# Kernel tuning notes

Hardware: AMD Instinct MI355X
Metric: run time of the kernel (lower is better)

The kernel has to match this reference:

```python
import jax, jax.numpy as jnp
import numpy as np

B, S, HID = 1, 2048, 7168
QLORA = 1536
NH = 32          # index_n_heads
HD = 128         # index_head_dim
ROPE = 64        # qk_rope_head_dim
TOPK = 512       # index_topk
EPS = 1e-6
NEG = -1e9       # finite mask value -> deterministic top-k (no -inf ties)


def _rope(x, cos, sin):
    # non-interleaved rotary: x [b,s,h,d]; cos/sin [s, d//2]
    half = x.shape[-1] // 2
    x1, x2 = x[..., :half], x[..., half:]
    c = cos[None, :, None, :]
    s = sin[None, :, None, :]
    return jnp.concatenate([x1 * c - x2 * s, x1 * s + x2 * c], axis=-1)


def setup_inputs() -> dict:
    key = jax.random.key(0)
    ks = jax.random.split(key, 8)
    x = jax.random.normal(ks[0], (B, S, HID), jnp.float32)
    qr = jax.random.normal(ks[1], (B, S, QLORA), jnp.float32)
    # rotary tables, theta=10000
    inv = 1.0 / (10000.0 ** (np.arange(0, ROPE, 2, dtype=np.float32) / ROPE))
    ang = np.arange(S, dtype=np.float32)[:, None] * inv[None, :]   # [S, ROPE//2]
    freqs_cos = jnp.asarray(np.cos(ang))
    freqs_sin = jnp.asarray(np.sin(ang))
    # causal additive mask [S, S], broadcasts over batch on [b,t,s]
    tri = jnp.tril(jnp.ones((S, S), jnp.bool_))
    mask = jnp.where(tri, 0.0, NEG).astype(jnp.float32)
    wq_b = jax.random.normal(ks[2], (QLORA, NH * HD), jnp.float32) / np.sqrt(QLORA)
    wk = jax.random.normal(ks[3], (HID, HD), jnp.float32) / np.sqrt(HID)
    k_norm_w = jnp.ones((HD,), jnp.float32)
    w_weights = jax.random.normal(ks[4], (HID, NH), jnp.float32) / np.sqrt(HID)
    return {"x": x, "qr": qr, "freqs_cos": freqs_cos, "freqs_sin": freqs_sin,
            "mask": mask, "wq_b": wq_b, "wk": wk, "k_norm_w": k_norm_w,
            "w_weights": w_weights}


def reference(x, qr, freqs_cos, freqs_sin, mask, wq_b, wk, k_norm_w, w_weights):
    b, s, _ = x.shape
    # queries
    q = (qr @ wq_b).reshape(b, s, NH, HD)
    q_pe, q_nope = q[..., :ROPE], q[..., ROPE:]
    q_pe = _rope(q_pe, freqs_cos, freqs_sin)
    q = jnp.concatenate([q_pe, q_nope], axis=-1)            # [b,s,NH,HD]
    # keys: project + RMSNorm + rope on first ROPE dims
    k = x @ wk                                              # [b,s,HD]
    var = jnp.mean(k * k, axis=-1, keepdims=True)
    k = k_norm_w * (k * jax.lax.rsqrt(var + EPS))
    k_pe, k_nope = k[..., :ROPE], k[..., ROPE:]
    k_pe = _rope(k_pe[:, :, None, :], freqs_cos, freqs_sin)[:, :, 0, :]
    k = jnp.concatenate([k_pe, k_nope], axis=-1)            # [b,s,HD]
    # per-head query weights
    weights = (x @ w_weights) * (NH ** -0.5) * (HD ** -0.5)  # [b,s,NH]
    # relu scores and per-head weighted reduction
    logits = jax.nn.relu(jnp.einsum('bthd,bsd->btsh', q, k))  # [b,t,s,NH]
    score = jnp.einsum('btsh,bth->bts', logits, weights) + mask
    # top-k token selection -> additive index mask
    topk_idx = jax.lax.top_k(score, min(TOPK, s))[1]          # [b,t,k]
    bi = jnp.arange(b)[:, None, None]
    ti = jnp.arange(s)[None, :, None]
    out = jnp.full((b, s, s), -jnp.inf, dtype=x.dtype)
    out = out.at[bi, ti, topk_idx].set(0.0)
    return out
```

## Files before the change

kernel.cpp:

```cpp
#include <hip/hip_runtime.h>
#include <hip/hip_bf16.h>
#include <math.h>

#define S_LEN 2048
#define HID   7168
#define QLORA 1536
#define NH    32
#define HD    128
#define T0    512
#define MROWS 1536
#define NEGV  -1000000000.0f
#define EPSV  1e-6f
#define NEG_FILL -3.0e38f
#define KSPLIT 16
#define KCHUNK 448

typedef __attribute__((ext_vector_type(8))) short bf16x8;
typedef __attribute__((ext_vector_type(4))) float f32x4;

__device__ __forceinline__ unsigned short f2bf(float x) {
    __hip_bfloat16 h = __float2bfloat16(x);
    union { __hip_bfloat16 h; unsigned short u; } cv; cv.h = h; return cv.u;
}
__device__ __forceinline__ float bf2f(short u) {
    return __uint_as_float(((unsigned)(unsigned short)u) << 16);
}
__device__ __forceinline__ void gload_lds16(const void* gsrc, void* ldst) {
    __builtin_amdgcn_global_load_lds(
        (const __attribute__((address_space(1))) void*)gsrc,
        (__attribute__((address_space(3))) void*)ldst,
        16, 0, 0);
}

__global__ __launch_bounds__(256) void transpose_wqb(
    const float* __restrict__ B, unsigned short* __restrict__ BT)
{
    __shared__ float tbuf[64][65];
    const int tid = threadIdx.x;
    const int n0 = blockIdx.x * 64;
    const int k0 = blockIdx.y * 64;
    {
        int r = tid >> 2, c0 = (tid & 3) * 16;
        const float* src = &B[(size_t)(k0 + r) * 4096 + n0 + c0];
        #pragma unroll
        for (int i = 0; i < 4; ++i) {
            float4 v = *(const float4*)(src + 4 * i);
            tbuf[r][c0 + 4 * i]     = v.x;
            tbuf[r][c0 + 4 * i + 1] = v.y;
            tbuf[r][c0 + 4 * i + 2] = v.z;
            tbuf[r][c0 + 4 * i + 3] = v.w;
        }
    }
    __syncthreads();
    {
        int nn = tid >> 2, ks = (tid & 3) * 16;
        bf16x8 p0, p1;
        #pragma unroll
        for (int j = 0; j < 8; ++j) {
            p0[j] = (short)f2bf(tbuf[ks + j][nn]);
            p1[j] = (short)f2bf(tbuf[ks + 8 + j][nn]);
        }
        unsigned short* dst = &BT[(size_t)(n0 + nn) * QLORA + k0 + ks];
        *(bf16x8*)dst       = p0;
        *(bf16x8*)(dst + 8) = p1;
    }
}

__global__ __launch_bounds__(256) void transpose_w(
    const float* __restrict__ wk, const float* __restrict__ ww,
    unsigned short* __restrict__ wbT)
{
    __shared__ float tbuf[64][33];
    const int tid = threadIdx.x;
    const int k0 = blockIdx.x * 64;
    const int nt = blockIdx.y;
    const float* src; int ld, nc0;
    if (nt < 4) { src = wk; ld = HD; nc0 = nt * 32; }
    else        { src = ww; ld = NH; nc0 = 0; }
    {
        int r = tid >> 2, c0 = (tid & 3) * 8;
        const float* sp = &src[(size_t)(k0 + r) * ld + nc0 + c0];
        #pragma unroll
        for (int i = 0; i < 2; ++i) {
            float4 v = *(const float4*)(sp + 4 * i);
            tbuf[r][c0 + 4 * i]     = v.x;
            tbuf[r][c0 + 4 * i + 1] = v.y;
            tbuf[r][c0 + 4 * i + 2] = v.z;
            tbuf[r][c0 + 4 * i + 3] = v.w;
        }
    }
    __syncthreads();
    {
        int nn = tid >> 3, ks = (tid & 7) * 8;
        bf16x8 p;
        #pragma unroll
        for (int j = 0; j < 8; ++j) p[j] = (short)f2bf(tbuf[ks + j][nn]);
        *(bf16x8*)&wbT[(size_t)(nt * 32 + nn) * HID + k0 + ks] = p;
    }
}

__global__ __launch_bounds__(256) void cast_qr(
    const float* __restrict__ qr, unsigned short* __restrict__ qrb)
{
    int idx = blockIdx.x * 256 + threadIdx.x;
    const float* src = qr + (size_t)T0 * QLORA + (size_t)idx * 8;
    float4 f0 = *(const float4*)src;
    float4 f1 = *(const float4*)(src + 4);
    bf16x8 p;
    p[0]=(short)f2bf(f0.x); p[1]=(short)f2bf(f0.y); p[2]=(short)f2bf(f0.z); p[3]=(short)f2bf(f0.w);
    p[4]=(short)f2bf(f1.x); p[5]=(short)f2bf(f1.y); p[6]=(short)f2bf(f1.z); p[7]=(short)f2bf(f1.w);
    *(bf16x8*)(qrb + (size_t)idx * 8) = p;
}

__global__ __launch_bounds__(256) void kw_gemm2(
    const float* __restrict__ x, const unsigned short* __restrict__ wbT,
    unsigned short* __restrict__ P)
{
    __shared__ char As[2][4096];
    __shared__ char Bs[2][10240];
    const int tid = threadIdx.x;
    const int bid = blockIdx.x;
    const int wg = (bid & 7) * 64 + (bid >> 3);
    const int kc = wg >> 5;
    const int m0 = (wg & 31) * 64;
    const int kbase = kc * KCHUNK;
    const int wv = tid >> 6, l = tid & 63, g = l >> 4, r15 = l & 15;
    const int ar = tid >> 2, asub = tid & 3;
    f32x4 acc[10] = {};
    float4 fa, fb;

#define LOAD_A(kt) do {                                                          \
        const float* ap = &x[(size_t)(m0 + ar) * HID + kbase + (kt) * 32 + asub * 8]; \
        fa = *(const float4*)ap;  fb = *(const float4*)(ap + 4);                 \
    } while (0)
#define WRITE_A(buf) do {                                                        \
        bf16x8 pk;                                                               \
        pk[0]=(short)f2bf(fa.x); pk[1]=(short)f2bf(fa.y);                        \
        pk[2]=(short)f2bf(fa.z); pk[3]=(short)f2bf(fa.w);                        \
        pk[4]=(short)f2bf(fb.x); pk[5]=(short)f2bf(fb.y);                        \
        pk[6]=(short)f2bf(fb.z); pk[7]=(short)f2bf(fb.w);                        \
        *(bf16x8*)(As[buf] + (ar << 6) + ((asub ^ ((ar >> 1) & 3)) << 4)) = pk;  \
    } while (0)
#define STAGE_B(buf, kt) do {                                                    \
        int k0_ = kbase + (kt) * 32;                                             \
        { int slot = (wv << 6) + l;                                              \
          int n_ = slot >> 2, sub_ = (slot & 3) ^ ((n_ >> 1) & 3);               \
          gload_lds16(wbT + (size_t)n_ * HID + k0_ + sub_ * 8,                   \
                      Bs[buf] + (wv << 10)); }                                   \
        { int slot = 256 + (wv << 6) + l;                                        \
          int n_ = slot >> 2, sub_ = (slot & 3) ^ ((n_ >> 1) & 3);               \
          gload_lds16(wbT + (size_t)n_ * HID + k0_ + sub_ * 8,                   \
                      Bs[buf] + 4096 + (wv << 10)); }                            \
        if (wv < 2) {                                                            \
          int slot = 512 + (wv << 6) + l;                                        \
          int n_ = slot >> 2, sub_ = (slot & 3) ^ ((n_ >> 1) & 3);               \
          gload_lds16(wbT + (size_t)n_ * HID + k0_ + sub_ * 8,                   \
                      Bs[buf] + 8192 + (wv << 10)); }                            \
    } while (0)

    LOAD_A(0);
    STAGE_B(0, 0);
    WRITE_A(0);
    __syncthreads();
    int cur = 0;
    for (int t = 0; t < 14; ++t) {
        if (t < 13) { LOAD_A(t + 1); STAGE_B(cur ^ 1, t + 1); }
        {
            char* Ab = As[cur];
            char* Bb = Bs[cur];
            int ra = (wv << 4) + r15;
            bf16x8 a = *(const bf16x8*)(Ab + (ra << 6) + ((g ^ ((ra >> 1) & 3)) << 4));
            #pragma unroll
            for (int fn = 0; fn < 10; ++fn) {
                int nb = (fn << 4) + r15;
                bf16x8 b = *(const bf16x8*)(Bb + (nb << 6) + ((g ^ ((nb >> 1) & 3)) << 4));
                acc[fn] = __builtin_amdgcn_mfma_f32_16x16x32_bf16(a, b, acc[fn], 0, 0, 0);
            }
        }
        if (t < 13) WRITE_A(cur ^ 1);
        __syncthreads();
        cur ^= 1;
    }
#undef LOAD_A
#undef WRITE_A
#undef STAGE_B
    #pragma unroll
    for (int fn = 0; fn < 10; ++fn)
        #pragma unroll
        for (int rr = 0; rr < 4; ++rr) {
            int row = m0 + (wv << 4) + (g << 2) + rr;
            P[((size_t)kc * S_LEN + row) * 160 + (fn << 4) + r15] = f2bf(acc[fn][rr]);
        }
}

__global__ __launch_bounds__(512) void kw_finish16(
    const unsigned short* __restrict__ P, const float* __restrict__ knw,
    const float* __restrict__ fcos, const float* __restrict__ fsin,
    unsigned short* __restrict__ Kf, float* __restrict__ W)
{
    __shared__ float res[16][160];
    __shared__ float rsq[16];
    const int tid = threadIdx.x;
    const int stile = blockIdx.x;
    const int row0 = stile * 16;
    const int r = tid >> 5, j = tid & 31;

    #pragma unroll
    for (int jj = 0; jj < 5; ++jj) {
        int c = j + 32 * jj;
        float s = 0.f;
        #pragma unroll
        for (int kc = 0; kc < KSPLIT; ++kc)
            s += bf2f((short)P[(size_t)(kc * S_LEN + row0 + r) * 160 + c]);
        res[r][c] = s;
    }
    __syncthreads();
    {
        float s2 = 0.f;
        #pragma unroll
        for (int cg = 0; cg < 4; ++cg) { float v = res[r][cg * 32 + j]; s2 += v * v; }
        #pragma unroll
        for (int off = 16; off > 0; off >>= 1) s2 += __shfl_xor(s2, off, 32);
        if (j == 0) rsq[r] = rsqrtf(s2 * (1.0f / 128.0f) + EPSV);
    }
    __syncthreads();
    {
        int rr = tid >> 5, h = tid & 31;
        W[(size_t)(row0 + rr) * NH + h] = res[rr][128 + h] * 0.015625f;
    }
    if (tid < 256) {
        int ks = tid >> 6, l = tid & 63;
        int row = l & 15, g = l >> 4;
        int t = row0 + row;
        float rs = rsq[row];
        bf16x8 pack;
        #pragma unroll
        for (int jj2 = 0; jj2 < 8; ++jj2) {
            int d = ks * 32 + 8 * g + jj2;
            float v;
            if (d < 32) {
                float a = res[row][d]      * rs * knw[d];
                float b = res[row][d + 32] * rs * knw[d + 32];
                v = a * fcos[(size_t)t * 32 + d] - b * fsin[(size_t)t * 32 + d];
            } else if (d < 64) {
                int jx = d - 32;
                float a = res[row][jx] * rs * knw[jx];
                float b = res[row][d]  * rs * knw[d];
                v = a * fsin[(size_t)t * 32 + jx] + b * fcos[(size_t)t * 32 + jx];
            } else {
                v = res[row][d] * rs * knw[d];
            }
            pack[jj2] = (short)f2bf(v);
        }
        *(bf16x8*)&Kf[(size_t)stile * 2048 + ks * 512 + l * 8] = pack;
    }
}

__global__ __launch_bounds__(256) void gemm_q2(
    const unsigned short* __restrict__ qrb, const unsigned short* __restrict__ wqbT,
    const float* __restrict__ fcos, const float* __restrict__ fsin,
    unsigned short* __restrict__ Qbu)
{
    __shared__ char lds[2][12288];
    const int tid = threadIdx.x;
    const int bid = blockIdx.x;
    const int wg = (bid & 7) * 96 + (bid >> 3);
    const int n0 = (wg / 24) * 128;
    const int m0 = (wg % 24) * 64;
    const int wv = tid >> 6, l = tid & 63, g = l >> 4, r15 = l & 15;
    const int lrow = l >> 2, lsub = l & 3;
    const int wm = wv >> 1, wn = wv & 1;
    f32x4 acc[2][4] = {};

#define STAGE_Q(buf, kt) do {                                                   \
        int k0_ = (kt) * 32;                                                    \
        { int row_ = wv * 16 + lrow; int gs_ = lsub ^ ((row_ >> 1) & 3);        \
          gload_lds16(qrb + (size_t)(m0 + row_) * QLORA + k0_ + gs_ * 8,        \
                      lds[buf] + (wv << 10)); }                                 \
        { int row_ = wv * 32 + lrow; int gs_ = lsub ^ ((row_ >> 1) & 3);        \
          gload_lds16(wqbT + (size_t)(n0 + row_) * QLORA + k0_ + gs_ * 8,       \
                      lds[buf] + 4096 + (wv << 11)); }                          \
        { int row_ = wv * 32 + 16 + lrow; int gs_ = lsub ^ ((row_ >> 1) & 3);   \
          gload_lds16(wqbT + (size_t)(n0 + row_) * QLORA + k0_ + gs_ * 8,       \
                      lds[buf] + 4096 + (wv << 11) + 1024); }                   \
    } while (0)

    STAGE_Q(0, 0);
    __syncthreads();
    int cur = 0;
    for (int t = 0; t < 48; ++t) {
        if (t + 1 < 48) STAGE_Q(cur ^ 1, t + 1);
        char* As = lds[cur];
        char* Bs = lds[cur] + 4096;
        bf16x8 a[2], b[4];
        #pragma unroll
        for (int fm = 0; fm < 2; ++fm) {
            int ra = wm * 32 + fm * 16 + r15;
            a[fm] = *(const bf16x8*)(As + (ra << 6) + ((g ^ ((ra >> 1) & 3)) << 4));
        }
        #pragma unroll
        for (int fn = 0; fn < 4; ++fn) {
            int nb = wn * 64 + fn * 16 + r15;
            b[fn] = *(const bf16x8*)(Bs + (nb << 6) + ((g ^ ((nb >> 1) & 3)) << 4));
        }
        #pragma unroll
        for (int fm = 0; fm < 2; ++fm)
            #pragma unroll
            for (int fn = 0; fn < 4; ++fn)
                acc[fm][fn] = __builtin_amdgcn_mfma_f32_16x16x32_bf16(a[fm], b[fn], acc[fm][fn], 0, 0, 0);
        __syncthreads();
        cur ^= 1;
    }
#undef STAGE_Q
    if (wn == 0) {
        #pragma unroll
        for (int fm = 0; fm < 2; ++fm)
            #pragma unroll
            for (int rr = 0; rr < 4; ++rr) {
                int t = T0 + m0 + wm * 32 + fm * 16 + 4 * g + rr;
                #pragma unroll
                for (int p = 0; p < 2; ++p) {
                    int jj = p * 16 + r15;
                    float c = fcos[(size_t)t * 32 + jj];
                    float s = fsin[(size_t)t * 32 + jj];
                    float a = acc[fm][p][rr], b = acc[fm][p + 2][rr];
                    acc[fm][p][rr]     = a * c - b * s;
                    acc[fm][p + 2][rr] = a * s + b * c;
                }
            }
    }
    #pragma unroll
    for (int fm = 0; fm < 2; ++fm)
        #pragma unroll
        for (int fn = 0; fn < 4; ++fn)
            #pragma unroll
            for (int rr = 0; rr < 4; ++rr) {
                int row = m0 + wm * 32 + fm * 16 + 4 * g + rr;
                int col = n0 + wn * 64 + fn * 16 + r15;
                Qbu[(size_t)row * 4096 + col] = f2bf(acc[fm][fn][rr]);
            }
}

__global__ __launch_bounds__(512, 2) void score_mfma3(
    const unsigned short* __restrict__ Qb, const unsigned short* __restrict__ Kf,
    const float* __restrict__ W, float* __restrict__ sc)
{
    __shared__ float ps[2][8][320];
    __shared__ float wl2[32][16];
    const int tid = threadIdx.x;
    const int tt  = 95 - blockIdx.x;
    const int sp  = blockIdx.y;
    const int t0  = T0 + 16 * tt;
    const int wv  = tid >> 6, l = tid & 63, g = l >> 4, r15 = l & 15;

    {
        int h = tid >> 4, gg = (tid >> 2) & 3, r = tid & 3;
        wl2[h][gg * 4 + r] = W[(size_t)(t0 + 4 * gg + r) * NH + h];
    }
    bf16x8 qf[4][4];
    {
        const unsigned short* qbase = Qb + (size_t)(16 * tt + r15) * 4096 + g * 8;
        #pragma unroll
        for (int hh = 0; hh < 4; ++hh)
            #pragma unroll
            for (int ks = 0; ks < 4; ++ks)
                qf[hh][ks] = *(const bf16x8*)(qbase + (4 * wv + hh) * 128 + ks * 32);
    }
    __syncthreads();

    const int nst = 33 + tt;
    bf16x8 kfc[4], kfn[4];
    if (sp < nst) {
        #pragma unroll
        for (int ks = 0; ks < 4; ++ks)
            kfc[ks] = *(const bf16x8*)&Kf[(size_t)sp * 2048 + ks * 512 + l * 8];
    }
    int pb = 0;
    for (int stile = sp; stile < nst; stile += 4) {
        if (stile + 4 < nst) {
            #pragma unroll
            for (int ks = 0; ks < 4; ++ks)
                kfn[ks] = *(const bf16x8*)&Kf[(size_t)(stile + 4) * 2048 + ks * 512 + l * 8];
        }
        f32x4 score = {0.f, 0.f, 0.f, 0.f};
        #pragma unroll
        for (int hh = 0; hh < 4; ++hh) {
            f32x4 acc = {0.f, 0.f, 0.f, 0.f};
            #pragma unroll
            for (int ks = 0; ks < 4; ++ks)
                acc = __builtin_amdgcn_mfma_f32_16x16x32_bf16(qf[hh][ks], kfc[ks], acc, 0, 0, 0);
            f32x4 w4 = *(const f32x4*)&wl2[4 * wv + hh][g * 4];
            #pragma unroll
            for (int r = 0; r < 4; ++r)
                score[r] += fmaxf(acc[r], 0.f) * w4[r];
        }
        #pragma unroll
        for (int r = 0; r < 4; ++r) ps[pb][wv][l * 5 + r] = score[r];
        __syncthreads();
        if (wv < 4) {
            float v = ps[pb][0][l * 5 + wv];
            #pragma unroll
            for (int w = 1; w < 8; ++w) v += ps[pb][w][l * 5 + wv];
            int t = t0 + 4 * g + wv;
            int s = stile * 16 + r15;
            sc[(size_t)(t - T0) * S_LEN + s] = (s <= t) ? v : NEGV;
        }
        #pragma unroll
        for (int ks = 0; ks < 4; ++ks) kfc[ks] = kfn[ks];
        pb ^= 1;
    }
}

__global__ __launch_bounds__(256) void topk_row(
    const float* __restrict__ sc, float* __restrict__ out)
{
    __shared__ float scl[S_LEN];
    __shared__ unsigned int hist[256];
    __shared__ unsigned int wtot[4];
    __shared__ unsigned int sh_prefix;
    __shared__ int sh_krem;
    const int tid = threadIdx.x;
    const int lane = tid & 63, wvi = tid >> 6;
    const int qrow = blockIdx.x;
    const int t = T0 + qrow;
    const float* srow = sc + (size_t)qrow * S_LEN;

    for (int i = tid; i < S_LEN; i += 256) {
        float v = srow[i];
        scl[i] = (i <= t) ? v : NEGV;
    }
    __syncthreads();
    unsigned int* u = (unsigned int*)scl;
    #pragma unroll
    for (int jj = 0; jj < 8; ++jj) {
        int i = tid * 8 + jj;
        unsigned int b = __float_as_uint(scl[i]);
        u[i] = (b & 0x80000000u) ? ~b : (b | 0x80000000u);
    }
    if (tid == 0) { sh_prefix = 0u; sh_krem = 512; }
    __syncthreads();

    #pragma unroll
    for (int pass = 0; pass < 4; ++pass) {
        const int shift = 24 - 8 * pass;
        hist[tid] = 0u;
        __syncthreads();
        unsigned int pfx = sh_prefix;
        #pragma unroll
        for (int jj = 0; jj < 8; ++jj) {
            unsigned int uv = u[tid * 8 + jj];
            bool ok = (pass == 0) || ((uv >> (shift + 8)) == (pfx >> (shift + 8)));
            if (ok) atomicAdd(&hist[(uv >> shift) & 255u], 1u);
        }
        __syncthreads();
        unsigned int v = hist[tid];
        unsigned int s = v;
        #pragma unroll
        for (int off = 1; off < 64; off <<= 1) {
            unsigned int t2 = __shfl_down(s, off, 64);
            if (lane + off < 64) s += t2;
        }
        if (lane == 0) wtot[wvi] = s;
        int krem = sh_krem;
        __syncthreads();
        unsigned int S = s;
        #pragma unroll
        for (int w = 0; w < 4; ++w)
            if (w > wvi) S += wtot[w];
        if ((int)S >= krem && (int)(S - v) < krem) {
            sh_krem = krem - (int)(S - v);
            sh_prefix = pfx | ((unsigned int)tid << shift);
        }
        __syncthreads();
    }

    const unsigned int uthr = sh_prefix;
    const int krem = sh_krem;
    int ec = 0;
    #pragma unroll
    for (int jj = 0; jj < 8; ++jj) ec += (u[tid * 8 + jj] == uthr) ? 1 : 0;
    unsigned int c = (unsigned int)ec;
    unsigned int p = c;
    #pragma unroll
    for (int off = 1; off < 64; off <<= 1) {
        unsigned int t2 = __shfl_up(p, off, 64);
        if (lane >= off) p += t2;
    }
    if (lane == 63) wtot[wvi] = p;
    __syncthreads();
    unsigned int add = 0;
    #pragma unroll
    for (int w = 0; w < 4; ++w)
        if (w < wvi) add += wtot[w];
    int base = (int)(p - c + add);

    float* orow = out + (size_t)t * S_LEN;
    float o[8];
    #pragma unroll
    for (int jj = 0; jj < 8; ++jj) {
        unsigned int uv = u[tid * 8 + jj];
        bool sel;
        if (uv > uthr) { sel = true; }
        else if (uv == uthr) { sel = (base < krem); base++; }
        else { sel = false; }
        o[jj] = sel ? 0.0f : NEG_FILL;
    }
    float4 o0 = {o[0], o[1], o[2], o[3]};
    float4 o1 = {o[4], o[5], o[6], o[7]};
    *(float4*)&orow[tid * 8]     = o0;
    *(float4*)&orow[tid * 8 + 4] = o1;
}

__global__ __launch_bounds__(256) void fill_low(float* __restrict__ out)
{
    int idx = blockIdx.x * 256 + threadIdx.x;
    if (idx >= (T0 * S_LEN) / 4) return;
    int col4 = idx & 511;
    float v = (col4 < 128) ? 0.0f : NEG_FILL;
    float4 o = {v, v, v, v};
    ((float4*)out)[idx] = o;
}

extern "C" void kernel_launch(void* const* d_in, const int* in_sizes, int n_in,
                              void* d_out, int out_size, void* d_ws, size_t ws_size,
                              hipStream_t stream)
{
    (void)in_sizes; (void)n_in; (void)out_size; (void)ws_size;
    const float* x    = (const float*)d_in[0];
    const float* qr   = (const float*)d_in[1];
    const float* fcos = (const float*)d_in[2];
    const float* fsin = (const float*)d_in[3];
    const float* wq_b = (const float*)d_in[5];
    const float* wk   = (const float*)d_in[6];
    const float* knw  = (const float*)d_in[7];
    const float* ww   = (const float*)d_in[8];
    float* out = (float*)d_out;
    char*  wsb = (char*)d_ws;

    unsigned short* Kf   = (unsigned short*)wsb;
    float*          W    = (float*)(wsb + 512 * 1024);
    char*           reg1 = wsb + 768 * 1024;
    char*           reg2 = reg1 + 12582912;
    unsigned short* wbT  = (unsigned short*)reg1;
    unsigned short* Qbu  = (unsigned short*)reg1;
    unsigned short* P    = (unsigned short*)reg2;
    unsigned short* wqbT = (unsigned short*)reg2;
    float*          sc   = (float*)reg2;
    unsigned short* qrb  = (unsigned short*)d_out;

    transpose_w   <<<dim3(112, 5), 256, 0, stream>>>(wk, ww, wbT);
    kw_gemm2      <<<512, 256,        0, stream>>>(x, wbT, P);
    kw_finish16   <<<128, 512,        0, stream>>>(P, knw, fcos, fsin, Kf, W);
    transpose_wqb <<<dim3(64, 24), 256, 0, stream>>>(wq_b, wqbT);
    cast_qr       <<<1152, 256,       0, stream>>>(qr, qrb);
    gemm_q2       <<<768, 256,        0, stream>>>(qrb, wqbT, fcos, fsin, Qbu);
    score_mfma3   <<<dim3(96, 4), 512,  0, stream>>>(Qbu, Kf, W, sc);
    topk_row      <<<MROWS, 256,      0, stream>>>(sc, out);
    fill_low      <<<(T0 * S_LEN / 4 + 255) / 256, 256, 0, stream>>>(out);
}
```

Baseline: 156.0 us.

## Fuse qr fp32-to-bf16 cast into Q GEMM and enlarge its M tile

Removes the separate cast_qr kernel. The Q projection GEMM now loads fp32 qr rows into registers, converts them to bf16 and writes them into swizzled LDS, overlapping this with the MFMA work of the current stage. The M tile also doubles to 128, giving a 128x128 block tile with 4x4 MFMA fragments per wave, which halves the grid and improves reuse of the B tile. The cost is more registers for the accumulators and the staged A values, plus synchronous global loads for A instead of async LDS loads.

```diff
diff --git a/kernel.cpp b/kernel.cpp
--- a/kernel.cpp
+++ b/kernel.cpp
@@ -97,19 +97,6 @@
         for (int j = 0; j < 8; ++j) p[j] = (short)f2bf(tbuf[ks + j][nn]);
         *(bf16x8*)&wbT[(size_t)(nt * 32 + nn) * HID + k0 + ks] = p;
     }
-}
-
-__global__ __launch_bounds__(256) void cast_qr(
-    const float* __restrict__ qr, unsigned short* __restrict__ qrb)
-{
-    int idx = blockIdx.x * 256 + threadIdx.x;
-    const float* src = qr + (size_t)T0 * QLORA + (size_t)idx * 8;
-    float4 f0 = *(const float4*)src;
-    float4 f1 = *(const float4*)(src + 4);
-    bf16x8 p;
-    p[0]=(short)f2bf(f0.x); p[1]=(short)f2bf(f0.y); p[2]=(short)f2bf(f0.z); p[3]=(short)f2bf(f0.w);
-    p[4]=(short)f2bf(f1.x); p[5]=(short)f2bf(f1.y); p[6]=(short)f2bf(f1.z); p[7]=(short)f2bf(f1.w);
-    *(bf16x8*)(qrb + (size_t)idx * 8) = p;
 }
 
 __global__ __launch_bounds__(256) void kw_gemm2(
@@ -256,68 +243,92 @@
     }
 }
 
-__global__ __launch_bounds__(256) void gemm_q2(
-    const unsigned short* __restrict__ qrb, const unsigned short* __restrict__ wqbT,
+__global__ __launch_bounds__(256) void gemm_q3(
+    const float* __restrict__ qr, const unsigned short* __restrict__ wqbT,
     const float* __restrict__ fcos, const float* __restrict__ fsin,
     unsigned short* __restrict__ Qbu)
 {
-    __shared__ char lds[2][12288];
+    __shared__ char As[2][8192];
+    __shared__ char Bs[2][8192];
     const int tid = threadIdx.x;
     const int bid = blockIdx.x;
-    const int wg = (bid & 7) * 96 + (bid >> 3);
-    const int n0 = (wg / 24) * 128;
-    const int m0 = (wg % 24) * 64;
+    const int wg = (bid & 7) * 48 + (bid >> 3);
+    const int n0 = (wg / 12) * 128;
+    const int m0 = (wg % 12) * 128;
     const int wv = tid >> 6, l = tid & 63, g = l >> 4, r15 = l & 15;
-    const int lrow = l >> 2, lsub = l & 3;
     const int wm = wv >> 1, wn = wv & 1;
-    f32x4 acc[2][4] = {};
-
-#define STAGE_Q(buf, kt) do {                                                   \
-        int k0_ = (kt) * 32;                                                    \
-        { int row_ = wv * 16 + lrow; int gs_ = lsub ^ ((row_ >> 1) & 3);        \
-          gload_lds16(qrb + (size_t)(m0 + row_) * QLORA + k0_ + gs_ * 8,        \
-                      lds[buf] + (wv << 10)); }                                 \
-        { int row_ = wv * 32 + lrow; int gs_ = lsub ^ ((row_ >> 1) & 3);        \
-          gload_lds16(wqbT + (size_t)(n0 + row_) * QLORA + k0_ + gs_ * 8,       \
-                      lds[buf] + 4096 + (wv << 11)); }                          \
-        { int row_ = wv * 32 + 16 + lrow; int gs_ = lsub ^ ((row_ >> 1) & 3);   \
-          gload_lds16(wqbT + (size_t)(n0 + row_) * QLORA + k0_ + gs_ * 8,       \
-                      lds[buf] + 4096 + (wv << 11) + 1024); }                   \
+    const int ar = tid >> 1, ah = tid & 1;
+    f32x4 acc[4][4] = {};
+    float4 fa, fb, fc, fd;
+
+#define LOAD_A3(kt) do {                                                         \
+        const float* ap = &qr[(size_t)(T0 + m0 + ar) * QLORA + (kt) * 32 + ah * 16]; \
+        fa = *(const float4*)ap;       fb = *(const float4*)(ap + 4);            \
+        fc = *(const float4*)(ap + 8); fd = *(const float4*)(ap + 12);           \
     } while (0)
-
-    STAGE_Q(0, 0);
+#define WRITE_A3(buf) do {                                                       \
+        bf16x8 p0, p1;                                                           \
+        p0[0]=(short)f2bf(fa.x); p0[1]=(short)f2bf(fa.y);                        \
+        p0[2]=(short)f2bf(fa.z); p0[3]=(short)f2bf(fa.w);                        \
+        p0[4]=(short)f2bf(fb.x); p0[5]=(short)f2bf(fb.y);                        \
+        p0[6]=(short)f2bf(fb.z); p0[7]=(short)f2bf(fb.w);                        \
+        p1[0]=(short)f2bf(fc.x); p1[1]=(short)f2bf(fc.y);                        \
+        p1[2]=(short)f2bf(fc.z); p1[3]=(short)f2bf(fc.w);                        \
+        p1[4]=(short)f2bf(fd.x); p1[5]=(short)f2bf(fd.y);                        \
+        p1[6]=(short)f2bf(fd.z); p1[7]=(short)f2bf(fd.w);                        \
+        int sw_ = (ar >> 1) & 3;                                                 \
+        *(bf16x8*)(As[buf] + (ar << 6) + (((2*ah    ) ^ sw_) << 4)) = p0;        \
+        *(bf16x8*)(As[buf] + (ar << 6) + (((2*ah + 1) ^ sw_) << 4)) = p1;        \
+    } while (0)
+#define STAGE_B3(buf, kt) do {                                                   \
+        int k0_ = (kt) * 32;                                                     \
+        { int slot = (wv << 6) + l;                                              \
+          int n_ = slot >> 2, sub_ = (slot & 3) ^ ((n_ >> 1) & 3);               \
+          gload_lds16(wqbT + (size_t)(n0 + n_) * QLORA + k0_ + sub_ * 8,         \
+                      Bs[buf] + (wv << 10)); }                                   \
+        { int slot = 256 + (wv << 6) + l;                                        \
+          int n_ = slot >> 2, sub_ = (slot & 3) ^ ((n_ >> 1) & 3);               \
+          gload_lds16(wqbT + (size_t)(n0 + n_) * QLORA + k0_ + sub_ * 8,         \
+                      Bs[buf] + 4096 + (wv << 10)); }                            \
+    } while (0)
+
+    LOAD_A3(0);
+    STAGE_B3(0, 0);
+    WRITE_A3(0);
     __syncthreads();
     int cur = 0;
     for (int t = 0; t < 48; ++t) {
-        if (t + 1 < 48) STAGE_Q(cur ^ 1, t + 1);
-        char* As = lds[cur];
-        char* Bs = lds[cur] + 4096;
-        bf16x8 a[2], b[4];
-        #pragma unroll
-        for (int fm = 0; fm < 2; ++fm) {
-            int ra = wm * 32 + fm * 16 + r15;
-            a[fm] = *(const bf16x8*)(As + (ra << 6) + ((g ^ ((ra >> 1) & 3)) << 4));
-        }
-        #pragma unroll
-        for (int fn = 0; fn < 4; ++fn) {
-            int nb = wn * 64 + fn * 16 + r15;
-            b[fn] = *(const bf16x8*)(Bs + (nb << 6) + ((g ^ ((nb >> 1) & 3)) << 4));
-        }
-        #pragma unroll
-        for (int fm = 0; fm < 2; ++fm)
-            #pragma unroll
-            for (int fn = 0; fn < 4; ++fn)
-                acc[fm][fn] = __builtin_amdgcn_mfma_f32_16x16x32_bf16(a[fm], b[fn], acc[fm][fn], 0, 0, 0);
+        if (t + 1 < 48) { LOAD_A3(t + 1); STAGE_B3(cur ^ 1, t + 1); }
+        {
+            char* Ab = As[cur];
+            char* Bb = Bs[cur];
+            bf16x8 a[4], b[4];
+            #pragma unroll
+            for (int f = 0; f < 4; ++f) {
+                int ra = wm * 64 + f * 16 + r15;
+                int nb = wn * 64 + f * 16 + r15;
+                a[f] = *(const bf16x8*)(Ab + (ra << 6) + ((g ^ ((ra >> 1) & 3)) << 4));
+                b[f] = *(const bf16x8*)(Bb + (nb << 6) + ((g ^ ((nb >> 1) & 3)) << 4));
+            }
+            #pragma unroll
+            for (int fm = 0; fm < 4; ++fm)
+                #pragma unroll
+                for (int fn = 0; fn < 4; ++fn)
+                    acc[fm][fn] = __builtin_amdgcn_mfma_f32_16x16x32_bf16(a[fm], b[fn], acc[fm][fn], 0, 0, 0);
+        }
+        if (t + 1 < 48) WRITE_A3(cur ^ 1);
         __syncthreads();
         cur ^= 1;
     }
-#undef STAGE_Q
+#undef LOAD_A3
+#undef WRITE_A3
+#undef STAGE_B3
     if (wn == 0) {
         #pragma unroll
-        for (int fm = 0; fm < 2; ++fm)
+        for (int fm = 0; fm < 4; ++fm)
             #pragma unroll
             for (int rr = 0; rr < 4; ++rr) {
-                int t = T0 + m0 + wm * 32 + fm * 16 + 4 * g + rr;
+                int t = T0 + m0 + wm * 64 + fm * 16 + 4 * g + rr;
                 #pragma unroll
                 for (int p = 0; p < 2; ++p) {
                     int jj = p * 16 + r15;
@@ -330,12 +341,12 @@
             }
     }
     #pragma unroll
-    for (int fm = 0; fm < 2; ++fm)
+    for (int fm = 0; fm < 4; ++fm)
         #pragma unroll
         for (int fn = 0; fn < 4; ++fn)
             #pragma unroll
             for (int rr = 0; rr < 4; ++rr) {
-                int row = m0 + wm * 32 + fm * 16 + 4 * g + rr;
+                int row = m0 + wm * 64 + fm * 16 + 4 * g + rr;
                 int col = n0 + wn * 64 + fn * 16 + r15;
                 Qbu[(size_t)row * 4096 + col] = f2bf(acc[fm][fn][rr]);
             }
@@ -546,14 +557,12 @@
     unsigned short* P    = (unsigned short*)reg2;
     unsigned short* wqbT = (unsigned short*)reg2;
     float*          sc   = (float*)reg2;
-    unsigned short* qrb  = (unsigned short*)d_out;
 
     transpose_w   <<<dim3(112, 5), 256, 0, stream>>>(wk, ww, wbT);
     kw_gemm2      <<<512, 256,        0, stream>>>(x, wbT, P);
     kw_finish16   <<<128, 512,        0, stream>>>(P, knw, fcos, fsin, Kf, W);
     transpose_wqb <<<dim3(64, 24), 256, 0, stream>>>(wq_b, wqbT);
-    cast_qr       <<<1152, 256,       0, stream>>>(qr, qrb);
-    gemm_q2       <<<768, 256,        0, stream>>>(qrb, wqbT, fcos, fsin, Qbu);
+    gemm_q3       <<<384, 256,        0, stream>>>(qr, wqbT, fcos, fsin, Qbu);
     score_mfma3   <<<dim3(96, 4), 512,  0, stream>>>(Qbu, Kf, W, sc);
     topk_row      <<<MROWS, 256,      0, stream>>>(sc, out);
     fill_low      <<<(T0 * S_LEN / 4 + 255) / 256, 256, 0, stream>>>(out);
```

Result: slower. 164.9 us (+5.7%).

## Replace LDS-staged Q GEMM with per-wave register double-buffered direct loads

Applied to the files above, without the earlier changes.

The Q projection GEMM no longer stages tiles through shared memory with barriers. Each wave now owns a 64x64 output tile and loads its MFMA operands straight from global memory into registers, double-buffered two k-steps deep. This is meant to remove __syncthreads and LDS traffic and give each wave more MFMA work per load. The cost is more register pressure, no operand sharing across waves (more global/L2 traffic), and less coalesced 16-byte row-strided loads. Rope is applied only on even 64-column tiles, which lines up with the head boundaries.

```diff
diff --git a/kernel.cpp b/kernel.cpp
--- a/kernel.cpp
+++ b/kernel.cpp
@@ -256,73 +256,65 @@
     }
 }
 
-__global__ __launch_bounds__(256) void gemm_q2(
+__global__ __launch_bounds__(384) void gemm_q4(
     const unsigned short* __restrict__ qrb, const unsigned short* __restrict__ wqbT,
     const float* __restrict__ fcos, const float* __restrict__ fsin,
     unsigned short* __restrict__ Qbu)
 {
-    __shared__ char lds[2][12288];
-    const int tid = threadIdx.x;
-    const int bid = blockIdx.x;
-    const int wg = (bid & 7) * 96 + (bid >> 3);
-    const int n0 = (wg / 24) * 128;
-    const int m0 = (wg % 24) * 64;
-    const int wv = tid >> 6, l = tid & 63, g = l >> 4, r15 = l & 15;
-    const int lrow = l >> 2, lsub = l & 3;
-    const int wm = wv >> 1, wn = wv & 1;
-    f32x4 acc[2][4] = {};
-
-#define STAGE_Q(buf, kt) do {                                                   \
-        int k0_ = (kt) * 32;                                                    \
-        { int row_ = wv * 16 + lrow; int gs_ = lsub ^ ((row_ >> 1) & 3);        \
-          gload_lds16(qrb + (size_t)(m0 + row_) * QLORA + k0_ + gs_ * 8,        \
-                      lds[buf] + (wv << 10)); }                                 \
-        { int row_ = wv * 32 + lrow; int gs_ = lsub ^ ((row_ >> 1) & 3);        \
-          gload_lds16(wqbT + (size_t)(n0 + row_) * QLORA + k0_ + gs_ * 8,       \
-                      lds[buf] + 4096 + (wv << 11)); }                          \
-        { int row_ = wv * 32 + 16 + lrow; int gs_ = lsub ^ ((row_ >> 1) & 3);   \
-          gload_lds16(wqbT + (size_t)(n0 + row_) * QLORA + k0_ + gs_ * 8,       \
-                      lds[buf] + 4096 + (wv << 11) + 1024); }                   \
-    } while (0)
-
-    STAGE_Q(0, 0);
-    __syncthreads();
-    int cur = 0;
-    for (int t = 0; t < 48; ++t) {
-        if (t + 1 < 48) STAGE_Q(cur ^ 1, t + 1);
-        char* As = lds[cur];
-        char* Bs = lds[cur] + 4096;
-        bf16x8 a[2], b[4];
-        #pragma unroll
-        for (int fm = 0; fm < 2; ++fm) {
-            int ra = wm * 32 + fm * 16 + r15;
-            a[fm] = *(const bf16x8*)(As + (ra << 6) + ((g ^ ((ra >> 1) & 3)) << 4));
-        }
-        #pragma unroll
-        for (int fn = 0; fn < 4; ++fn) {
-            int nb = wn * 64 + fn * 16 + r15;
-            b[fn] = *(const bf16x8*)(Bs + (nb << 6) + ((g ^ ((nb >> 1) & 3)) << 4));
-        }
-        #pragma unroll
-        for (int fm = 0; fm < 2; ++fm)
+    const int tid = threadIdx.x;
+    const int wv = tid / 64, l = tid & 63, g = l >> 4, r15 = l & 15;
+    const int wid = (blockIdx.x & 7) * 192 + (blockIdx.x >> 3) * 6 + wv;
+    const int tn = wid / 24, tm = wid % 24;
+    const int m0 = tm * 64, n0 = tn * 64;
+    const unsigned short* ab = qrb  + (size_t)(m0 + r15) * QLORA + g * 8;
+    const unsigned short* bb = wqbT + (size_t)(n0 + r15) * QLORA + g * 8;
+    f32x4 acc[4][4] = {};
+    bf16x8 aA[4], bA[4], aB[4], bB[4];
+
+    #pragma unroll
+    for (int f = 0; f < 4; ++f) {
+        aA[f] = *(const bf16x8*)(ab + (size_t)f * 16 * QLORA);
+        bA[f] = *(const bf16x8*)(bb + (size_t)f * 16 * QLORA);
+    }
+    for (int t = 0; t < 48; t += 2) {
+        {
+            int k1 = (t + 1) * 32;
+            #pragma unroll
+            for (int f = 0; f < 4; ++f) {
+                aB[f] = *(const bf16x8*)(ab + (size_t)f * 16 * QLORA + k1);
+                bB[f] = *(const bf16x8*)(bb + (size_t)f * 16 * QLORA + k1);
+            }
+        }
+        #pragma unroll
+        for (int fm = 0; fm < 4; ++fm)
             #pragma unroll
             for (int fn = 0; fn < 4; ++fn)
-                acc[fm][fn] = __builtin_amdgcn_mfma_f32_16x16x32_bf16(a[fm], b[fn], acc[fm][fn], 0, 0, 0);
-        __syncthreads();
-        cur ^= 1;
-    }
-#undef STAGE_Q
-    if (wn == 0) {
-        #pragma unroll
-        for (int fm = 0; fm < 2; ++fm)
+                acc[fm][fn] = __builtin_amdgcn_mfma_f32_16x16x32_bf16(aA[fm], bA[fn], acc[fm][fn], 0, 0, 0);
+        if (t + 2 < 48) {
+            int k2 = (t + 2) * 32;
+            #pragma unroll
+            for (int f = 0; f < 4; ++f) {
+                aA[f] = *(const bf16x8*)(ab + (size_t)f * 16 * QLORA + k2);
+                bA[f] = *(const bf16x8*)(bb + (size_t)f * 16 * QLORA + k2);
+            }
+        }
+        #pragma unroll
+        for (int fm = 0; fm < 4; ++fm)
+            #pragma unroll
+            for (int fn = 0; fn < 4; ++fn)
+                acc[fm][fn] = __builtin_amdgcn_mfma_f32_16x16x32_bf16(aB[fm], bB[fn], acc[fm][fn], 0, 0, 0);
+    }
+    if ((tn & 1) == 0) {
+        #pragma unroll
+        for (int fm = 0; fm < 4; ++fm)
             #pragma unroll
             for (int rr = 0; rr < 4; ++rr) {
-                int t = T0 + m0 + wm * 32 + fm * 16 + 4 * g + rr;
+                int t_ = T0 + m0 + fm * 16 + 4 * g + rr;
                 #pragma unroll
                 for (int p = 0; p < 2; ++p) {
                     int jj = p * 16 + r15;
-                    float c = fcos[(size_t)t * 32 + jj];
-                    float s = fsin[(size_t)t * 32 + jj];
+                    float c = fcos[(size_t)t_ * 32 + jj];
+                    float s = fsin[(size_t)t_ * 32 + jj];
                     float a = acc[fm][p][rr], b = acc[fm][p + 2][rr];
                     acc[fm][p][rr]     = a * c - b * s;
                     acc[fm][p + 2][rr] = a * s + b * c;
@@ -330,13 +322,13 @@
             }
     }
     #pragma unroll
-    for (int fm = 0; fm < 2; ++fm)
+    for (int fm = 0; fm < 4; ++fm)
         #pragma unroll
         for (int fn = 0; fn < 4; ++fn)
             #pragma unroll
             for (int rr = 0; rr < 4; ++rr) {
-                int row = m0 + wm * 32 + fm * 16 + 4 * g + rr;
-                int col = n0 + wn * 64 + fn * 16 + r15;
+                int row = m0 + fm * 16 + 4 * g + rr;
+                int col = n0 + fn * 16 + r15;
                 Qbu[(size_t)row * 4096 + col] = f2bf(acc[fm][fn][rr]);
             }
 }
@@ -553,7 +545,7 @@
     kw_finish16   <<<128, 512,        0, stream>>>(P, knw, fcos, fsin, Kf, W);
     transpose_wqb <<<dim3(64, 24), 256, 0, stream>>>(wq_b, wqbT);
     cast_qr       <<<1152, 256,       0, stream>>>(qr, qrb);
-    gemm_q2       <<<768, 256,        0, stream>>>(qrb, wqbT, fcos, fsin, Qbu);
+    gemm_q4       <<<256, 384,        0, stream>>>(qrb, wqbT, fcos, fsin, Qbu);
     score_mfma3   <<<dim3(96, 4), 512,  0, stream>>>(Qbu, Kf, W, sc);
     topk_row      <<<MROWS, 256,      0, stream>>>(sc, out);
     fill_low      <<<(T0 * S_LEN / 4 + 255) / 256, 256, 0, stream>>>(out);
```

New measurement: 187.1 us. 19.9% more time.
